# Kernel optimization log

Measured on AMD Instinct MI355X. Metric: run time of the kernel, lower is better.

Reference implementation:

```python
import jax, jax.numpy as jnp
import numpy as np

SEQ, B, I, H = 512, 64, 1024, 1024
P_DROP = 0.1

def setup_inputs() -> dict:
    key = jax.random.key(0)
    ks = jax.random.split(key, 6)
    x = jax.random.normal(ks[0], (SEQ, B, I), dtype=jnp.float32)
    # deterministic dropout keep-mask (1.0 = keep), Bernoulli(1-p)
    keep_mask = (jax.random.uniform(ks[1], (SEQ, B, H)) > P_DROP).astype(jnp.float32)
    s_in = 1.0 / np.sqrt(H)
    W_ih = jax.random.normal(ks[2], (4 * H, I), dtype=jnp.float32) * s_in
    W_hh = jax.random.normal(ks[3], (4 * H, H), dtype=jnp.float32) * s_in
    b_ih = jax.random.normal(ks[4], (4 * H,), dtype=jnp.float32) * s_in
    b_hh = jax.random.normal(ks[5], (4 * H,), dtype=jnp.float32) * s_in
    return {"x": x, "keep_mask": keep_mask, "W_ih": W_ih, "W_hh": W_hh,
            "b_ih": b_ih, "b_hh": b_hh, "training": 1}

def reference(x, keep_mask, W_ih, W_hh, b_ih, b_hh, training):
    # PyTorch LSTMCell: gates in i, f, g, o order; stepwise inverted dropout on h.
    scale = 1.0 / (1.0 - P_DROP) if training else 1.0
    Hh = W_hh.shape[1]

    def step(carry, inp):
        h, c = carry
        xt, mt = inp  # [B,I], [B,H]
        gates = xt @ W_ih.T + b_ih + h @ W_hh.T + b_hh  # [B,4H]
        i_g, f_g, g_g, o_g = jnp.split(gates, 4, axis=-1)
        i_g = jax.nn.sigmoid(i_g)
        f_g = jax.nn.sigmoid(f_g)
        g_g = jnp.tanh(g_g)
        o_g = jax.nn.sigmoid(o_g)
        c = f_g * c + i_g * g_g
        h = o_g * jnp.tanh(c)
        if training:
            h = h * mt * scale  # stepwise dropout, dropped h fed to next step
        return (h, c), None

    h0 = jnp.zeros((x.shape[1], Hh), dtype=x.dtype)
    c0 = jnp.zeros_like(h0)
    (h, _), _ = jax.lax.scan(step, (h0, c0), (x, keep_mask))
    return h  # [B, H] final (dropped) hidden state
```

## Files before the change

kernel.cpp:

```cpp
#include <hip/hip_runtime.h>
#include <hip/hip_bf16.h>

typedef __bf16 bf16x8 __attribute__((ext_vector_type(8)));
typedef float  f32x4  __attribute__((ext_vector_type(4)));
typedef unsigned short u16;
typedef unsigned int   u32;

#define SEQ   512
#define BATCH 64
#define INP   1024
#define HID   1024
#define NREC  64
#define NGRID 256

#define WC_OFF    0ull
#define HSEQ_OFF  (WC_OFF + 16777216ull)
#define BIAS_OFF  (HSEQ_OFF + 67239936ull)
#define FLAGS_OFF (BIAS_OFF + 16384ull)
#define XC_OFF    (FLAGS_OFF + 16384ull)
#define WS_NEED_XC (XC_OFF + 67108864ull)

__device__ __forceinline__ u16 f2bf(float f) {
    u32 u = __float_as_uint(f);
    u = (u + 0x7FFFu + ((u >> 16) & 1u)) >> 16;
    return (u16)u;
}

__device__ __forceinline__ bf16x8 ld8(const u16* p) {
    return *reinterpret_cast<const bf16x8*>(p);
}

__device__ __forceinline__ bf16x8 cvt8(const float* p) {
    float4 lo = *reinterpret_cast<const float4*>(p);
    float4 hi = *reinterpret_cast<const float4*>(p + 4);
    union { __hip_bfloat162 h2[4]; bf16x8 v; } u;
    u.h2[0] = __float22bfloat162_rn(float2{lo.x, lo.y});
    u.h2[1] = __float22bfloat162_rn(float2{lo.z, lo.w});
    u.h2[2] = __float22bfloat162_rn(float2{hi.x, hi.y});
    u.h2[3] = __float22bfloat162_rn(float2{hi.z, hi.w});
    return u.v;
}

__device__ __forceinline__ float sigmoidf_fast(float x) {
    return 1.0f / (1.0f + __expf(-x));
}
__device__ __forceinline__ float tanhf_fast(float x) {
    return 2.0f / (1.0f + __expf(-2.0f * x)) - 1.0f;
}

__global__ void lstm_prep(const float* __restrict__ wih,
                          const float* __restrict__ whh,
                          const float* __restrict__ bih,
                          const float* __restrict__ bhh,
                          const float* __restrict__ xf,
                          u16* __restrict__ wc, u16* __restrict__ hseq,
                          float* __restrict__ bias, u32* __restrict__ flags,
                          u16* __restrict__ xc, int do_x) {
    const long long NW = 8388608ll;
    const long long NB = 4096ll;
    const long long NH = 65536ll;
    const long long NF = 2080ll;
    const long long NX = do_x ? 33554432ll : 0ll;
    const long long total = NW + NB + NH + NF + NX;
    long long stride = (long long)gridDim.x * blockDim.x;
    for (long long i = (long long)blockIdx.x * blockDim.x + threadIdx.x;
         i < total; i += stride) {
        if (i < NW) {
            long long row = i >> 11;
            long long col = i & 2047;
            float v = (col < 1024) ? wih[row * 1024 + col]
                                   : whh[row * 1024 + (col - 1024)];
            wc[i] = f2bf(v);
        } else if (i < NW + NB) {
            long long j = i - NW;
            bias[j] = bih[j] + bhh[j];
        } else if (i < NW + NB + NH) {
            hseq[i - NW - NB] = 0;
        } else if (i < NW + NB + NH + NF) {
            flags[i - NW - NB - NH] = 0;
        } else {
            long long j = i - NW - NB - NH - NF;
            xc[j] = f2bf(xf[j]);
        }
    }
}

__global__ __launch_bounds__(256, 1) void lstm_rec(
    const float* __restrict__ x, const u16* __restrict__ xc,
    const u16* __restrict__ wc,
    const float* __restrict__ bias, const float* __restrict__ km,
    u16* __restrict__ hseq, float* __restrict__ out,
    u32* __restrict__ flags, const int* __restrict__ trainp) {

    __shared__ float part[4][4][BATCH][16];

    const int tid = threadIdx.x;

    if (blockIdx.x >= NREC) {
        volatile int* mb = (volatile int*)&part[0][0][0][0];
        if (tid == 0) *mb = 0;
        __syncthreads();
        union { u32 u[4]; bf16x8 v; } ja, jb;
        #pragma unroll
        for (int i = 0; i < 4; ++i) {
            ja.u[i] = (u32)tid * 2654435761u + i;
            jb.u[i] = (u32)tid * 40503u + 7u * i + 1u;
        }
        f32x4 hacc[8];
        #pragma unroll
        for (int j = 0; j < 8; ++j) hacc[j] = (f32x4){0.f, 0.f, 0.f, 0.f};
        const u32* done = flags + 2048;
        for (int chunk = 0; chunk < 4096; ++chunk) {
            #pragma unroll 1
            for (int it = 0; it < 256; ++it) {
                #pragma unroll
                for (int j = 0; j < 8; ++j)
                    hacc[j] = __builtin_amdgcn_mfma_f32_16x16x32_bf16(
                        ja.v, jb.v, hacc[j], 0, 0, 0);
            }
            if (tid < 64) {
                u32 d = __hip_atomic_load(done, __ATOMIC_RELAXED,
                                          __HIP_MEMORY_SCOPE_AGENT);
                if (d) *mb = 1;
            }
            if (*mb) break;
        }
        float s = 0.f;
        #pragma unroll
        for (int j = 0; j < 8; ++j)
            s += hacc[j][0] + hacc[j][1] + hacc[j][2] + hacc[j][3];
        asm volatile("" :: "v"(s));
        return;
    }

    const int w    = tid >> 6;
    const int lane = tid & 63;
    const int quad = lane >> 4;
    const int l16  = lane & 15;
    const int cu   = blockIdx.x;
    const int col0 = cu * 16;

    const int training = trainp[0];
    const float scale = training ? (1.0f / 0.9f) : 1.0f;

    const u16* wbase = wc + (size_t)(col0 + l16) * 2048 + (size_t)w * 256
                          + (size_t)quad * 8;

    const int cj2 = (tid & 7) * 2;
    const int cb0 = tid >> 3;
    float bi[4][2];
    #pragma unroll
    for (int g = 0; g < 4; ++g) {
        bi[g][0] = bias[g * 1024 + col0 + cj2];
        bi[g][1] = bias[g * 1024 + col0 + cj2 + 1];
    }

    float creg[2][2] = {{0.f, 0.f}, {0.f, 0.f}};

    #pragma unroll 1
    for (int t = 0; t < SEQ; ++t) {
        float2 kmv[2];
        kmv[0] = *reinterpret_cast<const float2*>(
            &km[(size_t)t * 65536 + (size_t)cb0 * 1024 + col0 + cj2]);
        kmv[1] = *reinterpret_cast<const float2*>(
            &km[(size_t)t * 65536 + (size_t)(cb0 + 32) * 1024 + col0 + cj2]);

        f32x4 acc[4][4];
        #pragma unroll
        for (int g = 0; g < 4; ++g)
            #pragma unroll
            for (int mt = 0; mt < 4; ++mt)
                acc[g][mt] = (f32x4){0.f, 0.f, 0.f, 0.f};

        if (xc != nullptr) {
            const u16* Arow = xc + (size_t)t * 65536
                                 + (size_t)l16 * 1024 + (size_t)w * 256
                                 + (size_t)quad * 8;
            #pragma unroll 4
            for (int kk = 0; kk < 8; ++kk) {
                bf16x8 afr[4], bfr[4];
                #pragma unroll
                for (int mt = 0; mt < 4; ++mt)
                    afr[mt] = ld8(Arow + (size_t)mt * 16 * 1024 + kk * 32);
                #pragma unroll
                for (int g = 0; g < 4; ++g)
                    bfr[g] = ld8(wbase + (size_t)g * 1024 * 2048 + kk * 32);
                #pragma unroll
                for (int g = 0; g < 4; ++g)
                    #pragma unroll
                    for (int mt = 0; mt < 4; ++mt)
                        acc[g][mt] = __builtin_amdgcn_mfma_f32_16x16x32_bf16(
                            afr[mt], bfr[g], acc[g][mt], 0, 0, 0);
            }
        } else {
            const float* Arow = x + (size_t)t * (BATCH * INP)
                                  + (size_t)l16 * 1024 + (size_t)w * 256
                                  + (size_t)quad * 8;
            #pragma unroll 4
            for (int kk = 0; kk < 8; ++kk) {
                bf16x8 afr[4], bfr[4];
                #pragma unroll
                for (int mt = 0; mt < 4; ++mt)
                    afr[mt] = cvt8(Arow + (size_t)mt * 16 * 1024 + kk * 32);
                #pragma unroll
                for (int g = 0; g < 4; ++g)
                    bfr[g] = ld8(wbase + (size_t)g * 1024 * 2048 + kk * 32);
                #pragma unroll
                for (int g = 0; g < 4; ++g)
                    #pragma unroll
                    for (int mt = 0; mt < 4; ++mt)
                        acc[g][mt] = __builtin_amdgcn_mfma_f32_16x16x32_bf16(
                            afr[mt], bfr[g], acc[g][mt], 0, 0, 0);
            }
        }

        if (t > 0) {
            const u32* fl = flags + ((u32)lane << 5);
            while (true) {
                u32 f = __hip_atomic_load(fl, __ATOMIC_RELAXED,
                                          __HIP_MEMORY_SCOPE_AGENT);
                if (__ballot((int)f >= t) == 0xFFFFFFFFFFFFFFFFull) break;
                __builtin_amdgcn_s_sleep(1);
            }
            asm volatile("" ::: "memory");
        }

        {
            const u16* Hrow = hseq + (size_t)t * 65536
                                   + (size_t)l16 * 1024 + (size_t)w * 256
                                   + (size_t)quad * 8;
            #pragma unroll 4
            for (int kk = 0; kk < 8; ++kk) {
                bf16x8 afr[4], bfr[4];
                #pragma unroll
                for (int mt = 0; mt < 4; ++mt)
                    afr[mt] = ld8(Hrow + (size_t)mt * 16 * 1024 + kk * 32);
                #pragma unroll
                for (int g = 0; g < 4; ++g)
                    bfr[g] = ld8(wbase + 1024 + (size_t)g * 1024 * 2048 + kk * 32);
                #pragma unroll
                for (int g = 0; g < 4; ++g)
                    #pragma unroll
                    for (int mt = 0; mt < 4; ++mt)
                        acc[g][mt] = __builtin_amdgcn_mfma_f32_16x16x32_bf16(
                            afr[mt], bfr[g], acc[g][mt], 0, 0, 0);
            }
        }

        #pragma unroll
        for (int g = 0; g < 4; ++g)
            #pragma unroll
            for (int mt = 0; mt < 4; ++mt)
                #pragma unroll
                for (int r = 0; r < 4; ++r)
                    part[w][g][mt * 16 + quad * 4 + r][l16] = acc[g][mt][r];

        __syncthreads();

        u16* hout = hseq + (size_t)(t + 1) * 65536;
        #pragma unroll
        for (int r = 0; r < 2; ++r) {
            int b = cb0 + 32 * r;
            float hv[2];
            #pragma unroll
            for (int c = 0; c < 2; ++c) {
                int j = cj2 + c;
                float gi = part[0][0][b][j] + part[1][0][b][j]
                         + part[2][0][b][j] + part[3][0][b][j] + bi[0][c];
                float gf = part[0][1][b][j] + part[1][1][b][j]
                         + part[2][1][b][j] + part[3][1][b][j] + bi[1][c];
                float gg = part[0][2][b][j] + part[1][2][b][j]
                         + part[2][2][b][j] + part[3][2][b][j] + bi[2][c];
                float go = part[0][3][b][j] + part[1][3][b][j]
                         + part[2][3][b][j] + part[3][3][b][j] + bi[3][c];

                float ig = sigmoidf_fast(gi);
                float fg = sigmoidf_fast(gf);
                float gt = tanhf_fast(gg);
                float og = sigmoidf_fast(go);

                float cv = fg * creg[r][c] + ig * gt;
                creg[r][c] = cv;
                float h = og * tanhf_fast(cv);
                if (training)
                    h = h * (c ? kmv[r].y : kmv[r].x) * scale;
                hv[c] = h;
            }
            int cidx = b * 1024 + col0 + cj2;
            u32 packed = (u32)f2bf(hv[0]) | ((u32)f2bf(hv[1]) << 16);
            __hip_atomic_store((u32*)(hout + cidx), packed,
                               __ATOMIC_RELAXED, __HIP_MEMORY_SCOPE_AGENT);
            if (t == SEQ - 1) {
                out[cidx]     = hv[0];
                out[cidx + 1] = hv[1];
            }
        }

        asm volatile("s_waitcnt vmcnt(0)" ::: "memory");
        __syncthreads();
        if (tid == 0) {
            __hip_atomic_store(flags + ((u32)cu << 5), (u32)(t + 1),
                               __ATOMIC_RELAXED, __HIP_MEMORY_SCOPE_AGENT);
        }
    }

    if (cu == 0 && tid == 0) {
        __hip_atomic_store(flags + 2048, 1u,
                           __ATOMIC_RELAXED, __HIP_MEMORY_SCOPE_AGENT);
    }
}

extern "C" void kernel_launch(void* const* d_in, const int* in_sizes, int n_in,
                              void* d_out, int out_size, void* d_ws, size_t ws_size,
                              hipStream_t stream) {
    const float* x   = (const float*)d_in[0];
    const float* km  = (const float*)d_in[1];
    const float* wih = (const float*)d_in[2];
    const float* whh = (const float*)d_in[3];
    const float* bih = (const float*)d_in[4];
    const float* bhh = (const float*)d_in[5];
    const int*   tr  = (const int*)d_in[6];
    float* out = (float*)d_out;

    char* ws = (char*)d_ws;
    u16*   wc    = (u16*)(ws + WC_OFF);
    u16*   hseq  = (u16*)(ws + HSEQ_OFF);
    float* bias  = (float*)(ws + BIAS_OFF);
    u32*   flags = (u32*)(ws + FLAGS_OFF);

    const int use_xc = (ws_size >= WS_NEED_XC) ? 1 : 0;
    u16* xc = use_xc ? (u16*)(ws + XC_OFF) : nullptr;

    lstm_prep<<<dim3(2048), dim3(256), 0, stream>>>(wih, whh, bih, bhh, x,
                                                    wc, hseq, bias, flags,
                                                    xc, use_xc);
    lstm_rec<<<dim3(NGRID), dim3(256), 0, stream>>>(x, xc, wc, bias, km, hseq,
                                                    out, flags, tr);
}
```

Before: 9.018 ms.

## Precompute input projection for all timesteps in a separate parallel GEMM kernel

Adds a kernel that computes x_t @ W_ih^T for every timestep up front, with full parallelism, and stores the fp32 gate pre-activations in workspace. The recurrent kernel then loads these per-step values and only runs the h @ W_hh^T MFMA loop, which shortens the serial critical path. The path is used only when the workspace holds about 512MB extra; otherwise the old bf16-x path runs. The cost is a large extra GEMM pass and heavy memory traffic for the precomputed gates.

```diff
diff --git a/kernel.cpp b/kernel.cpp
--- a/kernel.cpp
+++ b/kernel.cpp
@@ -17,8 +17,9 @@
 #define HSEQ_OFF  (WC_OFF + 16777216ull)
 #define BIAS_OFF  (HSEQ_OFF + 67239936ull)
 #define FLAGS_OFF (BIAS_OFF + 16384ull)
-#define XC_OFF    (FLAGS_OFF + 16384ull)
-#define WS_NEED_XC (XC_OFF + 67108864ull)
+#define XTRA_OFF  (FLAGS_OFF + 16384ull)
+#define WS_NEED_XC (XTRA_OFF + 67108864ull)
+#define WS_NEED_XG (XTRA_OFF + 536870912ull)
 
 __device__ __forceinline__ u16 f2bf(float f) {
     u32 u = __float_as_uint(f);
@@ -85,12 +86,64 @@
     }
 }
 
+__global__ __launch_bounds__(256, 1) void lstm_xg(
+    const float* __restrict__ x, const u16* __restrict__ wc,
+    float* __restrict__ xg) {
+    const int tid  = threadIdx.x;
+    const int w    = tid >> 6;
+    const int lane = tid & 63;
+    const int quad = lane >> 4;
+    const int l16  = lane & 15;
+    const int job  = blockIdx.x * 4 + w;
+    const int cu   = job & 63;
+    const int t    = job >> 6;
+    const int col0 = cu * 16;
+
+    const float* Abase = x + (size_t)t * 65536 + (size_t)l16 * 1024 + quad * 8;
+    const u16*   Bbase = wc + (size_t)(col0 + l16) * 2048 + quad * 8;
+
+    f32x4 acc[4][4];
+    #pragma unroll
+    for (int g = 0; g < 4; ++g)
+        #pragma unroll
+        for (int mt = 0; mt < 4; ++mt)
+            acc[g][mt] = (f32x4){0.f, 0.f, 0.f, 0.f};
+
+    #pragma unroll 4
+    for (int kk = 0; kk < 32; ++kk) {
+        bf16x8 afr[4], bfr[4];
+        #pragma unroll
+        for (int mt = 0; mt < 4; ++mt)
+            afr[mt] = cvt8(Abase + (size_t)mt * 16 * 1024 + kk * 32);
+        #pragma unroll
+        for (int g = 0; g < 4; ++g)
+            bfr[g] = ld8(Bbase + (size_t)g * 1024 * 2048 + kk * 32);
+        #pragma unroll
+        for (int g = 0; g < 4; ++g)
+            #pragma unroll
+            for (int mt = 0; mt < 4; ++mt)
+                acc[g][mt] = __builtin_amdgcn_mfma_f32_16x16x32_bf16(
+                    afr[mt], bfr[g], acc[g][mt], 0, 0, 0);
+    }
+
+    float* Obase = xg + (size_t)t * 262144 + (size_t)(quad * 4) * 4096
+                      + col0 + l16;
+    #pragma unroll
+    for (int g = 0; g < 4; ++g)
+        #pragma unroll
+        for (int mt = 0; mt < 4; ++mt)
+            #pragma unroll
+            for (int r = 0; r < 4; ++r)
+                Obase[(size_t)(mt * 16 + r) * 4096 + g * 1024] = acc[g][mt][r];
+}
+
 __global__ __launch_bounds__(256, 1) void lstm_rec(
     const float* __restrict__ x, const u16* __restrict__ xc,
     const u16* __restrict__ wc,
     const float* __restrict__ bias, const float* __restrict__ km,
     u16* __restrict__ hseq, float* __restrict__ out,
-    u32* __restrict__ flags, const int* __restrict__ trainp) {
+    u32* __restrict__ flags, const int* __restrict__ trainp,
+    const float* __restrict__ xg) {
 
     __shared__ float part[4][4][BATCH][16];
 
@@ -172,7 +225,21 @@
             for (int mt = 0; mt < 4; ++mt)
                 acc[g][mt] = (f32x4){0.f, 0.f, 0.f, 0.f};
 
-        if (xc != nullptr) {
+        float xgv[4][2][2];
+        if (xg != nullptr) {
+            const float* xgp = xg + (size_t)t * 262144;
+            #pragma unroll
+            for (int r = 0; r < 2; ++r) {
+                int b = cb0 + 32 * r;
+                #pragma unroll
+                for (int g = 0; g < 4; ++g) {
+                    float2 v = *reinterpret_cast<const float2*>(
+                        &xgp[(size_t)b * 4096 + g * 1024 + col0 + cj2]);
+                    xgv[g][r][0] = v.x;
+                    xgv[g][r][1] = v.y;
+                }
+            }
+        } else if (xc != nullptr) {
             const u16* Arow = xc + (size_t)t * 65536
                                  + (size_t)l16 * 1024 + (size_t)w * 256
                                  + (size_t)quad * 8;
@@ -258,6 +325,7 @@
         __syncthreads();
 
         u16* hout = hseq + (size_t)(t + 1) * 65536;
+        const int have_xg = (xg != nullptr);
         #pragma unroll
         for (int r = 0; r < 2; ++r) {
             int b = cb0 + 32 * r;
@@ -273,6 +341,12 @@
                          + part[2][2][b][j] + part[3][2][b][j] + bi[2][c];
                 float go = part[0][3][b][j] + part[1][3][b][j]
                          + part[2][3][b][j] + part[3][3][b][j] + bi[3][c];
+                if (have_xg) {
+                    gi += xgv[0][r][c];
+                    gf += xgv[1][r][c];
+                    gg += xgv[2][r][c];
+                    go += xgv[3][r][c];
+                }
 
                 float ig = sigmoidf_fast(gi);
                 float fg = sigmoidf_fast(gf);
@@ -328,12 +402,16 @@
     float* bias  = (float*)(ws + BIAS_OFF);
     u32*   flags = (u32*)(ws + FLAGS_OFF);
 
-    const int use_xc = (ws_size >= WS_NEED_XC) ? 1 : 0;
-    u16* xc = use_xc ? (u16*)(ws + XC_OFF) : nullptr;
+    const int use_xg = (ws_size >= WS_NEED_XG) ? 1 : 0;
+    const int use_xc = (!use_xg && ws_size >= WS_NEED_XC) ? 1 : 0;
+    float* xgp = use_xg ? (float*)(ws + XTRA_OFF) : nullptr;
+    u16*   xc  = use_xc ? (u16*)(ws + XTRA_OFF) : nullptr;
 
     lstm_prep<<<dim3(2048), dim3(256), 0, stream>>>(wih, whh, bih, bhh, x,
                                                     wc, hseq, bias, flags,
                                                     xc, use_xc);
+    if (use_xg)
+        lstm_xg<<<dim3(8192), dim3(256), 0, stream>>>(x, wc, xgp);
     lstm_rec<<<dim3(NGRID), dim3(256), 0, stream>>>(x, xc, wc, bias, km, hseq,
-                                                    out, flags, tr);
-}
+                                                    out, flags, tr, xgp);
+}
```

New measurement: 9.048 ms. About the same (+0.3%).
